# Performance work log

Measured on AMD Instinct MI355X. Metric: run time of the kernel, lower is better.

Reference implementation:

```python
import jax, jax.numpy as jnp
import numpy as np

V, E, G = 25000, 50000, 1024
D_IN, E_IN, D, EH = 74, 12, 64, 128
STEPS, S2S, L, NT = 6, 6, 3, 1


def setup_inputs() -> dict:
    key = jax.random.key(0)
    ks = jax.random.split(key, 20)
    p = lambda k, shp: (jax.random.normal(k, shp, jnp.float32) * 0.05)
    return {
        "node_feats": jax.random.normal(ks[0], (V, D_IN), jnp.float32),
        "edge_feats": jax.random.normal(ks[1], (E, E_IN), jnp.float32),
        "src": jax.random.randint(ks[2], (E,), 0, V),
        "dst": jax.random.randint(ks[3], (E,), 0, V),
        "node2graph": jnp.sort(jax.random.randint(ks[4], (V,), 0, G)),
        "W_proj": p(ks[5], (D_IN, D)), "b_proj": jnp.zeros((D,), jnp.float32),
        "W_e1": p(ks[6], (E_IN, EH)), "b_e1": jnp.zeros((EH,), jnp.float32),
        "W_e2": p(ks[7], (EH, D * D)), "b_e2": jnp.zeros((D * D,), jnp.float32),
        "b_conv": jnp.zeros((D,), jnp.float32),
        "gru_W_ih": p(ks[8], (3 * D, D)), "gru_W_hh": p(ks[9], (3 * D, D)),
        "gru_b_ih": jnp.zeros((3 * D,), jnp.float32), "gru_b_hh": jnp.zeros((3 * D,), jnp.float32),
        "lstm_W_ih0": p(ks[10], (4 * D, 2 * D)), "lstm_W_hh0": p(ks[11], (4 * D, D)),
        "lstm_b_ih0": jnp.zeros((4 * D,), jnp.float32), "lstm_b_hh0": jnp.zeros((4 * D,), jnp.float32),
        "lstm_W_ih_r": p(ks[12], (L - 1, 4 * D, D)), "lstm_W_hh_r": p(ks[13], (L - 1, 4 * D, D)),
        "lstm_b_ih_r": jnp.zeros((L - 1, 4 * D), jnp.float32), "lstm_b_hh_r": jnp.zeros((L - 1, 4 * D), jnp.float32),
        "W1": p(ks[14], (2 * D, D)), "b1": jnp.zeros((D,), jnp.float32),
        "bn_gamma": jnp.ones((D,), jnp.float32), "bn_beta": jnp.zeros((D,), jnp.float32),
        "bn_mean": jnp.zeros((D,), jnp.float32), "bn_var": jnp.ones((D,), jnp.float32),
        "W2": p(ks[15], (D, 4 * NT)), "b2": jnp.zeros((4 * NT,), jnp.float32),
    }


def reference(node_feats, edge_feats, src, dst, node2graph,
              W_proj, b_proj, W_e1, b_e1, W_e2, b_e2, b_conv,
              gru_W_ih, gru_W_hh, gru_b_ih, gru_b_hh,
              lstm_W_ih0, lstm_W_hh0, lstm_b_ih0, lstm_b_hh0,
              lstm_W_ih_r, lstm_W_hh_r, lstm_b_ih_r, lstm_b_hh_r,
              W1, b1, bn_gamma, bn_beta, bn_mean, bn_var, W2, b2):
    # --- MPNNGNN: project + ReLU, then NNConv(sum) + ReLU + GRU, x STEPS ---
    h = jax.nn.relu(node_feats @ W_proj + b_proj)                       # (V, D)
    # edge network: per-edge (D,D) mixing matrix (edge_feats constant across steps)
    We = (jax.nn.relu(edge_feats @ W_e1 + b_e1) @ W_e2 + b_e2).reshape(E, D, D)

    def mp_step(hh, _):
        m = jnp.einsum('ed,edo->eo', hh[src], We)                       # per-edge message
        agg = jax.ops.segment_sum(m, dst, num_segments=V) + b_conv      # NNConv sum + bias
        x = jax.nn.relu(agg)
        gi = x @ gru_W_ih.T + gru_b_ih                                  # GRU (torch gate order r,z,n)
        gh = hh @ gru_W_hh.T + gru_b_hh
        ir, iz, inn = jnp.split(gi, 3, axis=-1)
        hr, hz, hn = jnp.split(gh, 3, axis=-1)
        r = jax.nn.sigmoid(ir + hr)
        z = jax.nn.sigmoid(iz + hz)
        n = jnp.tanh(inn + r * hn)
        return (1.0 - z) * n + z * hh, None

    h, _ = jax.lax.scan(mp_step, h, None, length=STEPS)

    # --- Set2Set readout ---
    q_star = jnp.zeros((G, 2 * D), h.dtype)
    hs = jnp.zeros((L, G, D), h.dtype)
    cs = jnp.zeros((L, G, D), h.dtype)
    for _ in range(S2S):
        x = q_star
        nh, nc = [], []
        for l in range(L):                                              # stacked LSTM, seq len 1
            Wih = lstm_W_ih0 if l == 0 else lstm_W_ih_r[l - 1]
            Whh = lstm_W_hh0 if l == 0 else lstm_W_hh_r[l - 1]
            bih = lstm_b_ih0 if l == 0 else lstm_b_ih_r[l - 1]
            bhh = lstm_b_hh0 if l == 0 else lstm_b_hh_r[l - 1]
            gates = x @ Wih.T + bih + hs[l] @ Whh.T + bhh               # torch order i,f,g,o
            i, f, g, o = jnp.split(gates, 4, axis=-1)
            c = jax.nn.sigmoid(f) * cs[l] + jax.nn.sigmoid(i) * jnp.tanh(g)
            hc = jax.nn.sigmoid(o) * jnp.tanh(c)
            nh.append(hc); nc.append(c)
            x = hc
        hs, cs = jnp.stack(nh), jnp.stack(nc)
        q = x                                                           # (G, D)
        e = jnp.sum(h * q[node2graph], axis=-1)                         # (V,) attention logits
        emax = jax.lax.stop_gradient(jax.ops.segment_max(e, node2graph, num_segments=G))
        emax = jnp.where(jnp.isfinite(emax), emax, 0.0)
        ez = jnp.exp(e - emax[node2graph])                              # per-graph softmax
        denom = jax.ops.segment_sum(ez, node2graph, num_segments=G)
        alpha = ez / jnp.maximum(denom[node2graph], 1e-12)
        readout = jax.ops.segment_sum(h * alpha[:, None], node2graph, num_segments=G)
        q_star = jnp.concatenate([q, readout], axis=-1)                 # (G, 2D)

    # --- evidential head: Linear + ReLU + BatchNorm(eval) + Linear ---
    h1 = jax.nn.relu(q_star @ W1 + b1)
    hbn = bn_gamma * (h1 - bn_mean) * jax.lax.rsqrt(bn_var + 1e-5) + bn_beta
    out = hbn @ W2 + b2                                                 # (G, 4*NT)
    means, logl, loga, logb = jnp.split(out, 4, axis=1)
    MINV = 1e-6
    lam = jax.nn.softplus(logl) + MINV
    alp = jax.nn.softplus(loga) + MINV + 1.0
    bet = jax.nn.softplus(logb) + MINV
    return jnp.stack([means, lam, alp, bet], axis=2).reshape(out.shape)
```

## Files before the change

### kernel.cpp

```cpp
#include <hip/hip_runtime.h>
#include <stdint.h>

#define V_N 25000
#define E_N 50000
#define G_N 1024
#define DIN 74
#define EIN 12
#define NSTEPS 6
#define NS2S 6
#define MPAD 50176

typedef unsigned int u32;
typedef unsigned short u16;
typedef __attribute__((ext_vector_type(8))) short bf16x8v;
typedef __attribute__((ext_vector_type(4))) float f32x4v;

typedef __attribute__((address_space(3))) void lds_void;
typedef __attribute__((address_space(1))) void gbl_void;

__device__ __forceinline__ void gload_lds16(const void* g, void* l) {
  __builtin_amdgcn_global_load_lds((gbl_void*)g, (lds_void*)l, 16, 0, 0);
}

__device__ __forceinline__ u16 f2bf(float f) {
  u32 u = __float_as_uint(f);
  u = (u + 0x7fffu + ((u >> 16) & 1u)) >> 16;
  return (u16)u;
}
__device__ __forceinline__ u32 pack2bf(float lo, float hi) {
  return (u32)f2bf(lo) | ((u32)f2bf(hi) << 16);
}
__device__ __forceinline__ float bflo(u32 w){ return __uint_as_float(w << 16); }
__device__ __forceinline__ float bfhi(u32 w){ return __uint_as_float(w & 0xffff0000u); }
__device__ __forceinline__ float bf2f(u16 v){ return __uint_as_float(((u32)v) << 16); }
__device__ __forceinline__ float sigf(float x){ return 1.f/(1.f + expf(-x)); }
__device__ __forceinline__ float splusf(float x){ return fmaxf(x, 0.f) + log1pf(expf(-fabsf(x))); }

__global__ void prep_kernel(const float* gWih, const float* gWhh,
                            const float* lWih0, const float* lWhh0,
                            const float* lWihr, const float* lWhhr,
                            const float* We2,
                            float* gWihT, float* gWhhT,
                            u32* TW40, u32* TU40, u32* TW4r, u32* TU4r,
                            u16* WbT) {
  int idx = blockIdx.x * 256 + threadIdx.x;
  if (idx < 12288) { int d = idx / 192, r = idx % 192; gWihT[idx] = gWih[r*64 + d]; return; }
  idx -= 12288;
  if (idx < 12288) { int d = idx / 192, r = idx % 192; gWhhT[idx] = gWhh[r*64 + d]; return; }
  idx -= 12288;
  if (idx < 16384) { int q = idx >> 2, j = idx & 3; int k8 = q >> 8, r = q & 255;
                     TW40[idx] = pack2bf(lWih0[r*128 + k8*8 + 2*j], lWih0[r*128 + k8*8 + 2*j + 1]); return; }
  idx -= 16384;
  if (idx < 8192)  { int q = idx >> 2, j = idx & 3; int k8 = q >> 8, r = q & 255;
                     TU40[idx] = pack2bf(lWhh0[r*64 + k8*8 + 2*j], lWhh0[r*64 + k8*8 + 2*j + 1]); return; }
  idx -= 8192;
  if (idx < 16384) { int l = idx >> 13, rem = idx & 8191; int q = rem >> 2, j = rem & 3;
                     int k8 = q >> 8, r = q & 255;
                     TW4r[idx] = pack2bf(lWihr[l*16384 + r*64 + k8*8 + 2*j],
                                         lWihr[l*16384 + r*64 + k8*8 + 2*j + 1]); return; }
  idx -= 16384;
  if (idx < 16384) { int l = idx >> 13, rem = idx & 8191; int q = rem >> 2, j = rem & 3;
                     int k8 = q >> 8, r = q & 255;
                     TU4r[idx] = pack2bf(lWhhr[l*16384 + r*64 + k8*8 + 2*j],
                                         lWhhr[l*16384 + r*64 + k8*8 + 2*j + 1]); return; }
  idx -= 16384;
  { int n = idx / 128, k = idx % 128; WbT[idx] = f2bf(We2[k*4096 + n]); }
}

__global__ void proj_kernel(const float* nf, const float* Wp, const float* bp, float* h) {
  int v = blockIdx.x * 4 + (threadIdx.x >> 6);
  int o = threadIdx.x & 63;
  if (v >= V_N) return;
  float acc = bp[o];
  const float* row = nf + (size_t)v * DIN;
  #pragma unroll 2
  for (int d = 0; d < DIN; ++d) acc += row[d] * Wp[d*64 + o];
  h[(size_t)v*64 + o] = fmaxf(acc, 0.f);
}

__global__ void edgenet_kernel(const float* ef, const float* W1, const float* b1, u16* zb) {
  int e = blockIdx.x * 2 + (threadIdx.x >> 7);
  int k = threadIdx.x & 127;
  float acc = 0.f;
  if (e < E_N) {
    acc = b1[k];
    const float* row = ef + (size_t)e * EIN;
    #pragma unroll
    for (int i = 0; i < EIN; ++i) acc += row[i] * W1[i*128 + k];
    acc = fmaxf(acc, 0.f);
  }
  zb[(size_t)e*128 + k] = f2bf(acc);
}

__global__ __launch_bounds__(256) void fusedmsg_kernel(const u16* zb, const u16* WbT, const float* be2,
                                                       const float* h, const int* src, const int* dst,
                                                       float* agg) {
  __shared__ __align__(16) u16 Bs[2][8192];
  __shared__ u16 hS[128][66];
  __shared__ float beS[4096];
  int t = threadIdx.x;
  int e0 = blockIdx.x * 128;
  int w = t >> 6, lane = t & 63;
  int l16 = lane & 15, lh = lane >> 4;

  #pragma unroll
  for (int it = 0; it < 16; ++it) beS[it * 256 + t] = be2[it * 256 + t];

  for (int it = 0; it < 32; ++it) {
    int idx = it * 256 + t;
    int el = idx >> 6, d = idx & 63;
    int e = e0 + el;
    int sv = (e < E_N) ? src[e] : 0;
    hS[el][d] = f2bf(h[(size_t)sv * 64 + d]);
  }

  bf16x8v af[2][4];
  #pragma unroll
  for (int rf = 0; rf < 2; ++rf)
    #pragma unroll
    for (int ks = 0; ks < 4; ++ks)
      af[rf][ks] = *(const bf16x8v*)(zb + (size_t)(e0 + w*32 + rf*16 + l16)*128 + ks*32 + lh*8);

  {
    const char* Bg = (const char*)WbT;
    char* Bl = (char*)Bs[0];
    #pragma unroll
    for (int it = 0; it < 4; ++it) {
      int f = it * 256 + t;
      int r = f >> 4, s = f & 15;
      int gc = s ^ (r & 7);
      gload_lds16(Bg + r*256 + gc*16, Bl + (size_t)(f & ~63) * 16);
    }
  }
  __syncthreads();

  float macc[2][4][4];
  #pragma unroll
  for (int rf = 0; rf < 2; ++rf)
    #pragma unroll
    for (int of = 0; of < 4; ++of)
      #pragma unroll
      for (int r = 0; r < 4; ++r) macc[rf][of][r] = 0.f;

  for (int d = 0; d < 64; ++d) {
    int buf = d & 1;
    if (d < 63) {
      const char* Bg = (const char*)WbT + (size_t)(d + 1) * 16384;
      char* Bl = (char*)Bs[buf ^ 1];
      #pragma unroll
      for (int it = 0; it < 4; ++it) {
        int f = it * 256 + t;
        int r = f >> 4, s = f & 15;
        int gc = s ^ (r & 7);
        gload_lds16(Bg + r*256 + gc*16, Bl + (size_t)(f & ~63) * 16);
      }
    }
    float hv[2][4];
    #pragma unroll
    for (int rf = 0; rf < 2; ++rf)
      #pragma unroll
      for (int r = 0; r < 4; ++r)
        hv[rf][r] = bf2f(hS[w*32 + rf*16 + lh*4 + r][d]);

    const char* Bb = (const char*)Bs[buf];
    #pragma unroll
    for (int of = 0; of < 4; ++of) {
      float bias = beS[d*64 + of*16 + l16];
      f32x4v c0 = (f32x4v){bias, bias, bias, bias};
      f32x4v c1 = c0;
      #pragma unroll
      for (int ks = 0; ks < 4; ++ks) {
        int brow = of*16 + l16;
        int cb = ks*4 + lh;
        bf16x8v bf = *(const bf16x8v*)(Bb + brow*256 + ((cb ^ (brow & 7)) << 4));
        c0 = __builtin_amdgcn_mfma_f32_16x16x32_bf16(af[0][ks], bf, c0, 0, 0, 0);
        c1 = __builtin_amdgcn_mfma_f32_16x16x32_bf16(af[1][ks], bf, c1, 0, 0, 0);
      }
      #pragma unroll
      for (int r = 0; r < 4; ++r) {
        macc[0][of][r] += hv[0][r] * c0[r];
        macc[1][of][r] += hv[1][r] * c1[r];
      }
    }
    __syncthreads();
  }

  #pragma unroll
  for (int rf = 0; rf < 2; ++rf)
    #pragma unroll
    for (int r = 0; r < 4; ++r) {
      int row = w*32 + rf*16 + lh*4 + r;
      int e = e0 + row;
      if (e < E_N) {
        int dv = dst[e];
        #pragma unroll
        for (int of = 0; of < 4; ++of)
          atomicAdd(&agg[(size_t)dv*64 + of*16 + l16], macc[rf][of][r]);
      }
    }
}

__global__ void gru_kernel(const float* aggc, const float* bconv, const float* WihT, const float* WhhT,
                           const float* bih, const float* bhh, float* h, float* aggz) {
  int wbase = (blockIdx.x * 4 + (threadIdx.x >> 6)) * 4;
  int o = threadIdx.x & 63;
  float xv[4], hv[4];
  #pragma unroll
  for (int n = 0; n < 4; ++n) {
    int v = wbase + n;
    if (v < V_N) { xv[n] = fmaxf(aggc[(size_t)v*64 + o] + bconv[o], 0.f); hv[n] = h[(size_t)v*64 + o]; }
    else { xv[n] = 0.f; hv[n] = 0.f; }
  }
  float ar[4] = {0,0,0,0}, az[4] = {0,0,0,0}, an[4] = {0,0,0,0};
  float br[4] = {0,0,0,0}, bz[4] = {0,0,0,0}, bn2[4] = {0,0,0,0};
  #pragma unroll 4
  for (int d = 0; d < 64; ++d) {
    float wr = WihT[d*192 + o], wz = WihT[d*192 + 64 + o], wn = WihT[d*192 + 128 + o];
    float ur = WhhT[d*192 + o], uz = WhhT[d*192 + 64 + o], un = WhhT[d*192 + 128 + o];
    #pragma unroll
    for (int n = 0; n < 4; ++n) {
      float xd = __shfl(xv[n], d);
      float hd = __shfl(hv[n], d);
      ar[n] += xd*wr; az[n] += xd*wz; an[n] += xd*wn;
      br[n] += hd*ur; bz[n] += hd*uz; bn2[n] += hd*un;
    }
  }
  float b_r = bih[o] + bhh[o], b_z = bih[64+o] + bhh[64+o];
  float bin = bih[128+o], bhn = bhh[128+o];
  #pragma unroll
  for (int n = 0; n < 4; ++n) {
    int v = wbase + n;
    if (v >= V_N) continue;
    float r  = sigf(ar[n] + br[n] + b_r);
    float z  = sigf(az[n] + bz[n] + b_z);
    float nn = tanhf(an[n] + bin + r*(bn2[n] + bhn));
    h[(size_t)v*64 + o] = (1.f - z)*nn + z*hv[n];
    aggz[(size_t)v*64 + o] = 0.f;
  }
}

__global__ void gstart_kernel(const int* n2g, int* gstart) {
  int g = blockIdx.x * 256 + threadIdx.x;
  if (g > G_N) return;
  int lo = 0, hi = V_N;
  while (lo < hi) { int mid = (lo + hi) >> 1; if (n2g[mid] < g) lo = mid + 1; else hi = mid; }
  gstart[g] = lo;
}

__global__ __launch_bounds__(256) void s2s_kernel(const float* h, const int* gstart,
    const uint4* TW40, const uint4* TU40, const uint4* TW4r, const uint4* TU4r,
    const float* bih0, const float* bhh0, const float* bihr, const float* bhhr,
    float* qstar) {
  __shared__ float sq[2][128];
  __shared__ float sx[2][128];
  __shared__ float shs[2][3][64], scs[2][3][64];
  __shared__ float sg[2][256];
  __shared__ float sred[2][2][66];
  int tt = threadIdx.x;
  int g0blk = blockIdx.x * 2;
  int w = tt >> 6, lane = tt & 63;
  int gsl = w >> 1, wsub = w & 1;
  int nstart = gstart[g0blk + gsl], nend = gstart[g0blk + gsl + 1];

  if (tt < 256) { ((float*)sq)[tt] = 0.f; }
  for (int i = tt; i < 384; i += 256) { ((float*)shs)[i] = 0.f; ((float*)scs)[i] = 0.f; }
  __syncthreads();

  for (int iter = 0; iter < NS2S; ++iter) {
    ((float*)sx)[tt] = ((float*)sq)[tt];
    __syncthreads();

    for (int l = 0; l < 3; ++l) {
      const uint4* TW = (l == 0) ? TW40 : TW4r + (size_t)(l-1) * 2048;
      const uint4* TU = (l == 0) ? TU40 : TU4r + (size_t)(l-1) * 2048;
      const float* bi = (l == 0) ? bih0 : bihr + (l-1)*256;
      const float* bh = (l == 0) ? bhh0 : bhhr + (l-1)*256;
      float bsum = bi[tt] + bh[tt];
      float acc0 = bsum, acc1 = bsum;
      if (l == 0) {
        #pragma unroll
        for (int k8 = 0; k8 < 16; ++k8) {
          uint4 u = TW[k8*256 + tt];
          const float4 xa0 = *(const float4*)&sx[0][k8*8];
          const float4 xb0 = *(const float4*)&sx[0][k8*8 + 4];
          const float4 xa1 = *(const float4*)&sx[1][k8*8];
          const float4 xb1 = *(const float4*)&sx[1][k8*8 + 4];
          float w0=bflo(u.x),w1=bfhi(u.x),w2=bflo(u.y),w3=bfhi(u.y);
          float w4=bflo(u.z),w5=bfhi(u.z),w6=bflo(u.w),w7=bfhi(u.w);
          acc0 += xa0.x*w0 + xa0.y*w1 + xa0.z*w2 + xa0.w*w3
                + xb0.x*w4 + xb0.y*w5 + xb0.z*w6 + xb0.w*w7;
          acc1 += xa1.x*w0 + xa1.y*w1 + xa1.z*w2 + xa1.w*w3
                + xb1.x*w4 + xb1.y*w5 + xb1.z*w6 + xb1.w*w7;
        }
      } else {
        #pragma unroll
        for (int k8 = 0; k8 < 8; ++k8) {
          uint4 u = TW[k8*256 + tt];
          const float4 xa0 = *(const float4*)&sx[0][k8*8];
          const float4 xb0 = *(const float4*)&sx[0][k8*8 + 4];
          const float4 xa1 = *(const float4*)&sx[1][k8*8];
          const float4 xb1 = *(const float4*)&sx[1][k8*8 + 4];
          float w0=bflo(u.x),w1=bfhi(u.x),w2=bflo(u.y),w3=bfhi(u.y);
          float w4=bflo(u.z),w5=bfhi(u.z),w6=bflo(u.w),w7=bfhi(u.w);
          acc0 += xa0.x*w0 + xa0.y*w1 + xa0.z*w2 + xa0.w*w3
                + xb0.x*w4 + xb0.y*w5 + xb0.z*w6 + xb0.w*w7;
          acc1 += xa1.x*w0 + xa1.y*w1 + xa1.z*w2 + xa1.w*w3
                + xb1.x*w4 + xb1.y*w5 + xb1.z*w6 + xb1.w*w7;
        }
      }
      #pragma unroll
      for (int k8 = 0; k8 < 8; ++k8) {
        uint4 u = TU[k8*256 + tt];
        const float4 ha0 = *(const float4*)&shs[0][l][k8*8];
        const float4 hb0 = *(const float4*)&shs[0][l][k8*8 + 4];
        const float4 ha1 = *(const float4*)&shs[1][l][k8*8];
        const float4 hb1 = *(const float4*)&shs[1][l][k8*8 + 4];
        float w0=bflo(u.x),w1=bfhi(u.x),w2=bflo(u.y),w3=bfhi(u.y);
        float w4=bflo(u.z),w5=bfhi(u.z),w6=bflo(u.w),w7=bfhi(u.w);
        acc0 += ha0.x*w0 + ha0.y*w1 + ha0.z*w2 + ha0.w*w3
              + hb0.x*w4 + hb0.y*w5 + hb0.z*w6 + hb0.w*w7;
        acc1 += ha1.x*w0 + ha1.y*w1 + ha1.z*w2 + ha1.w*w3
              + hb1.x*w4 + hb1.y*w5 + hb1.z*w6 + hb1.w*w7;
      }
      sg[0][tt] = acc0; sg[1][tt] = acc1;
      __syncthreads();
      if (tt < 128) {
        int gq = tt >> 6, r = tt & 63;
        float gv_i = sg[gq][r], gv_f = sg[gq][64+r], gv_g = sg[gq][128+r], gv_o = sg[gq][192+r];
        float c = sigf(gv_f)*scs[gq][l][r] + sigf(gv_i)*tanhf(gv_g);
        float hc = sigf(gv_o)*tanhf(c);
        scs[gq][l][r] = c; shs[gq][l][r] = hc; sx[gq][r] = hc;
      }
      __syncthreads();
    }

    {
      float q_l = sx[gsl][lane];
      float lmax = -3.4e38f;
      int i = nstart + wsub;
      for (; i + 2 < nend; i += 4) {
        float h0 = h[(size_t)i*64 + lane];
        float h1 = h[(size_t)(i+2)*64 + lane];
        float v0 = h0 * q_l, v1 = h1 * q_l;
        #pragma unroll
        for (int off = 32; off; off >>= 1) { v0 += __shfl_xor(v0, off); v1 += __shfl_xor(v1, off); }
        lmax = fmaxf(lmax, fmaxf(v0, v1));
      }
      if (i < nend) {
        float h0 = h[(size_t)i*64 + lane];
        float v0 = h0 * q_l;
        #pragma unroll
        for (int off = 32; off; off >>= 1) v0 += __shfl_xor(v0, off);
        lmax = fmaxf(lmax, v0);
      }
      if (lane == 0) sred[gsl][wsub][64] = lmax;
      __syncthreads();
      float gmax = fmaxf(sred[gsl][0][64], sred[gsl][1][64]);
      float lsum = 0.f, accv = 0.f;
      i = nstart + wsub;
      for (; i + 2 < nend; i += 4) {
        float h0 = h[(size_t)i*64 + lane];
        float h1 = h[(size_t)(i+2)*64 + lane];
        float v0 = h0 * q_l, v1 = h1 * q_l;
        #pragma unroll
        for (int off = 32; off; off >>= 1) { v0 += __shfl_xor(v0, off); v1 += __shfl_xor(v1, off); }
        float e0 = expf(v0 - gmax), e1 = expf(v1 - gmax);
        lsum += e0 + e1; accv += e0*h0 + e1*h1;
      }
      if (i < nend) {
        float h0 = h[(size_t)i*64 + lane];
        float v0 = h0 * q_l;
        #pragma unroll
        for (int off = 32; off; off >>= 1) v0 += __shfl_xor(v0, off);
        float e0 = expf(v0 - gmax);
        lsum += e0; accv += e0*h0;
      }
      sred[gsl][wsub][lane] = accv;
      if (lane == 0) sred[gsl][wsub][65] = lsum;
      __syncthreads();
      if (tt < 128) {
        int gq = tt >> 6, r = tt & 63;
        float den = sred[gq][0][65] + sred[gq][1][65];
        float ro = (sred[gq][0][r] + sred[gq][1][r]) / fmaxf(den, 1e-12f);
        sq[gq][r] = sx[gq][r];
        sq[gq][64 + r] = ro;
      }
      __syncthreads();
    }
  }

  qstar[(size_t)g0blk * 128 + tt] = ((float*)sq)[tt];
}

__global__ void head_kernel(const float* qstar, const float* W1, const float* b1,
                            const float* gma, const float* gbe, const float* gme, const float* gva,
                            const float* W2, const float* b2, float* out) {
  __shared__ float hb[4][64];
  int wslot = threadIdx.x >> 6;
  int g = blockIdx.x * 4 + wslot;
  int o = threadIdx.x & 63;
  float acc = b1[o];
  const float* q = qstar + (size_t)g * 128;
  #pragma unroll 4
  for (int k = 0; k < 128; ++k) acc += q[k] * W1[k*64 + o];
  acc = fmaxf(acc, 0.f);
  float hbn = gma[o] * (acc - gme[o]) * rsqrtf(gva[o] + 1e-5f) + gbe[o];
  hb[wslot][o] = hbn;
  __syncthreads();
  if (o < 4) {
    float v = b2[o];
    #pragma unroll 8
    for (int k = 0; k < 64; ++k) v += hb[wslot][k] * W2[k*4 + o];
    float res;
    if (o == 0) res = v;
    else { res = splusf(v) + 1e-6f; if (o == 2) res += 1.f; }
    out[(size_t)g*4 + o] = res;
  }
}

extern "C" void kernel_launch(void* const* d_in, const int* in_sizes, int n_in,
                              void* d_out, int out_size, void* d_ws, size_t ws_size,
                              hipStream_t stream) {
  const float* node_feats = (const float*)d_in[0];
  const float* edge_feats = (const float*)d_in[1];
  const int*   src        = (const int*)d_in[2];
  const int*   dst        = (const int*)d_in[3];
  const int*   n2g        = (const int*)d_in[4];
  const float* W_proj = (const float*)d_in[5];
  const float* b_proj = (const float*)d_in[6];
  const float* W_e1   = (const float*)d_in[7];
  const float* b_e1   = (const float*)d_in[8];
  const float* W_e2   = (const float*)d_in[9];
  const float* b_e2   = (const float*)d_in[10];
  const float* b_conv = (const float*)d_in[11];
  const float* gru_W_ih = (const float*)d_in[12];
  const float* gru_W_hh = (const float*)d_in[13];
  const float* gru_b_ih = (const float*)d_in[14];
  const float* gru_b_hh = (const float*)d_in[15];
  const float* lstm_W_ih0 = (const float*)d_in[16];
  const float* lstm_W_hh0 = (const float*)d_in[17];
  const float* lstm_b_ih0 = (const float*)d_in[18];
  const float* lstm_b_hh0 = (const float*)d_in[19];
  const float* lstm_W_ih_r = (const float*)d_in[20];
  const float* lstm_W_hh_r = (const float*)d_in[21];
  const float* lstm_b_ih_r = (const float*)d_in[22];
  const float* lstm_b_hh_r = (const float*)d_in[23];
  const float* W1 = (const float*)d_in[24];
  const float* b1 = (const float*)d_in[25];
  const float* bn_gamma = (const float*)d_in[26];
  const float* bn_beta  = (const float*)d_in[27];
  const float* bn_mean  = (const float*)d_in[28];
  const float* bn_var   = (const float*)d_in[29];
  const float* W2 = (const float*)d_in[30];
  const float* b2 = (const float*)d_in[31];

  char* ws = (char*)d_ws;
  size_t off = 0;
  auto alloc = [&](size_t n) { size_t c = off; off += (n + 255) & ~(size_t)255; return c; };
  u16*   zb     = (u16*)  (ws + alloc((size_t)MPAD * 128 * 2));
  float* h      = (float*)(ws + alloc((size_t)V_N * 64 * 4));
  float* agg    = (float*)(ws + alloc((size_t)V_N * 64 * 4));
  u16*   WbT    = (u16*)  (ws + alloc((size_t)4096 * 128 * 2));
  float* gWihT  = (float*)(ws + alloc(12288 * 4));
  float* gWhhT  = (float*)(ws + alloc(12288 * 4));
  u32*   TW40   = (u32*)  (ws + alloc(16384 * 4));
  u32*   TU40   = (u32*)  (ws + alloc(8192 * 4));
  u32*   TW4r   = (u32*)  (ws + alloc(16384 * 4));
  u32*   TU4r   = (u32*)  (ws + alloc(16384 * 4));
  int*   gstart = (int*)  (ws + alloc(1025 * 4));
  float* qstar  = (float*)(ws + alloc((size_t)G_N * 128 * 4));
  (void)in_sizes; (void)n_in; (void)out_size; (void)ws_size;

  prep_kernel<<<2368, 256, 0, stream>>>(gru_W_ih, gru_W_hh, lstm_W_ih0, lstm_W_hh0,
                                        lstm_W_ih_r, lstm_W_hh_r, W_e2,
                                        gWihT, gWhhT, TW40, TU40, TW4r, TU4r, WbT);
  proj_kernel<<<6250, 256, 0, stream>>>(node_feats, W_proj, b_proj, h);
  edgenet_kernel<<<MPAD / 2, 256, 0, stream>>>(edge_feats, W_e1, b_e1, zb);
  hipMemsetAsync(agg, 0, (size_t)V_N * 64 * 4, stream);

  for (int st = 0; st < NSTEPS; ++st) {
    fusedmsg_kernel<<<MPAD / 128, 256, 0, stream>>>(zb, WbT, b_e2, h, src, dst, agg);
    gru_kernel<<<1563, 256, 0, stream>>>(agg, b_conv, gWihT, gWhhT, gru_b_ih, gru_b_hh, h, agg);
  }

  gstart_kernel<<<5, 256, 0, stream>>>(n2g, gstart);
  s2s_kernel<<<512, 256, 0, stream>>>(h, gstart, (const uint4*)TW40, (const uint4*)TU40,
                                      (const uint4*)TW4r, (const uint4*)TU4r,
                                      lstm_b_ih0, lstm_b_hh0, lstm_b_ih_r, lstm_b_hh_r, qstar);
  head_kernel<<<256, 256, 0, stream>>>(qstar, W1, b1, bn_gamma, bn_beta, bn_mean, bn_var,
                                       W2, b2, (float*)d_out);
}
```

Before: 1.140 ms.

## Rewrite Set2Set LSTM as single-wavefront-per-graph kernel with shuffle broadcasts

The Set2Set kernel now runs one 64-lane wavefront per graph instead of a 256-thread block covering two graphs. Each lane computes all four LSTM gates for its own hidden unit, so gate activations stay in registers. The input vector is broadcast with __shfl instead of through LDS, which removes every __syncthreads. LSTM weights are repacked in prep as gate-interleaved bf16 pairs indexed [k][o], and the biases are pre-summed. The trade-off is less parallelism for the attention loop over nodes and a longer serial chain of 64-step dot products per lane, which raises per-wave latency.

```diff
diff --git a/kernel.cpp b/kernel.cpp
--- a/kernel.cpp
+++ b/kernel.cpp
@@ -39,32 +39,59 @@
 __global__ void prep_kernel(const float* gWih, const float* gWhh,
                             const float* lWih0, const float* lWhh0,
                             const float* lWihr, const float* lWhhr,
+                            const float* lb_ih0, const float* lb_hh0,
+                            const float* lb_ihr, const float* lb_hhr,
                             const float* We2,
                             float* gWihT, float* gWhhT,
-                            u32* TW40, u32* TU40, u32* TW4r, u32* TU4r,
-                            u16* WbT) {
+                            uint2* T0W, uint2* T0U, uint2* TrW, uint2* TrU,
+                            float4* bs4, u16* WbT) {
   int idx = blockIdx.x * 256 + threadIdx.x;
   if (idx < 12288) { int d = idx / 192, r = idx % 192; gWihT[idx] = gWih[r*64 + d]; return; }
   idx -= 12288;
   if (idx < 12288) { int d = idx / 192, r = idx % 192; gWhhT[idx] = gWhh[r*64 + d]; return; }
   idx -= 12288;
-  if (idx < 16384) { int q = idx >> 2, j = idx & 3; int k8 = q >> 8, r = q & 255;
-                     TW40[idx] = pack2bf(lWih0[r*128 + k8*8 + 2*j], lWih0[r*128 + k8*8 + 2*j + 1]); return; }
-  idx -= 16384;
-  if (idx < 8192)  { int q = idx >> 2, j = idx & 3; int k8 = q >> 8, r = q & 255;
-                     TU40[idx] = pack2bf(lWhh0[r*64 + k8*8 + 2*j], lWhh0[r*64 + k8*8 + 2*j + 1]); return; }
+  if (idx < 8192) {
+    int k = idx >> 6, o = idx & 63;
+    T0W[idx] = (uint2){ pack2bf(lWih0[o*128 + k],        lWih0[(64+o)*128 + k]),
+                        pack2bf(lWih0[(128+o)*128 + k],  lWih0[(192+o)*128 + k]) };
+    return;
+  }
   idx -= 8192;
-  if (idx < 16384) { int l = idx >> 13, rem = idx & 8191; int q = rem >> 2, j = rem & 3;
-                     int k8 = q >> 8, r = q & 255;
-                     TW4r[idx] = pack2bf(lWihr[l*16384 + r*64 + k8*8 + 2*j],
-                                         lWihr[l*16384 + r*64 + k8*8 + 2*j + 1]); return; }
-  idx -= 16384;
-  if (idx < 16384) { int l = idx >> 13, rem = idx & 8191; int q = rem >> 2, j = rem & 3;
-                     int k8 = q >> 8, r = q & 255;
-                     TU4r[idx] = pack2bf(lWhhr[l*16384 + r*64 + k8*8 + 2*j],
-                                         lWhhr[l*16384 + r*64 + k8*8 + 2*j + 1]); return; }
-  idx -= 16384;
-  { int n = idx / 128, k = idx % 128; WbT[idx] = f2bf(We2[k*4096 + n]); }
+  if (idx < 4096) {
+    int k = idx >> 6, o = idx & 63;
+    T0U[idx] = (uint2){ pack2bf(lWhh0[o*64 + k],        lWhh0[(64+o)*64 + k]),
+                        pack2bf(lWhh0[(128+o)*64 + k],  lWhh0[(192+o)*64 + k]) };
+    return;
+  }
+  idx -= 4096;
+  if (idx < 8192) {
+    int l = idx >> 12, rem = idx & 4095;
+    int k = rem >> 6, o = rem & 63;
+    const float* W = lWihr + l*16384;
+    TrW[idx] = (uint2){ pack2bf(W[o*64 + k],        W[(64+o)*64 + k]),
+                        pack2bf(W[(128+o)*64 + k],  W[(192+o)*64 + k]) };
+    return;
+  }
+  idx -= 8192;
+  if (idx < 8192) {
+    int l = idx >> 12, rem = idx & 4095;
+    int k = rem >> 6, o = rem & 63;
+    const float* W = lWhhr + l*16384;
+    TrU[idx] = (uint2){ pack2bf(W[o*64 + k],        W[(64+o)*64 + k]),
+                        pack2bf(W[(128+o)*64 + k],  W[(192+o)*64 + k]) };
+    return;
+  }
+  idx -= 8192;
+  if (idx < 192) {
+    int l = idx >> 6, o = idx & 63;
+    const float* bi = (l == 0) ? lb_ih0 : lb_ihr + (l-1)*256;
+    const float* bh = (l == 0) ? lb_hh0 : lb_hhr + (l-1)*256;
+    bs4[idx] = (float4){ bi[o] + bh[o], bi[64+o] + bh[64+o],
+                         bi[128+o] + bh[128+o], bi[192+o] + bh[192+o] };
+    return;
+  }
+  idx -= 192;
+  if (idx < 524288) { int n = idx / 128, k = idx % 128; WbT[idx] = f2bf(We2[k*4096 + n]); }
 }
 
 __global__ void proj_kernel(const float* nf, const float* Wp, const float* bp, float* h) {
@@ -247,149 +274,119 @@
   gstart[g] = lo;
 }
 
-__global__ __launch_bounds__(256) void s2s_kernel(const float* h, const int* gstart,
-    const uint4* TW40, const uint4* TU40, const uint4* TW4r, const uint4* TU4r,
-    const float* bih0, const float* bhh0, const float* bihr, const float* bhhr,
-    float* qstar) {
-  __shared__ float sq[2][128];
-  __shared__ float sx[2][128];
-  __shared__ float shs[2][3][64], scs[2][3][64];
-  __shared__ float sg[2][256];
-  __shared__ float sred[2][2][66];
-  int tt = threadIdx.x;
-  int g0blk = blockIdx.x * 2;
-  int w = tt >> 6, lane = tt & 63;
-  int gsl = w >> 1, wsub = w & 1;
-  int nstart = gstart[g0blk + gsl], nend = gstart[g0blk + gsl + 1];
-
-  if (tt < 256) { ((float*)sq)[tt] = 0.f; }
-  for (int i = tt; i < 384; i += 256) { ((float*)shs)[i] = 0.f; ((float*)scs)[i] = 0.f; }
-  __syncthreads();
+__global__ __launch_bounds__(64) void s2s_kernel(const float* h, const int* gstart,
+    const uint2* T0W, const uint2* T0U, const uint2* TrW, const uint2* TrU,
+    const float4* bs4, float* qstar) {
+  int lane = threadIdx.x;
+  int g = blockIdx.x;
+  int ns = gstart[g], ne = gstart[g + 1];
+  float xq = 0.f, xr = 0.f;
+  float hs0 = 0.f, hs1 = 0.f, hs2 = 0.f;
+  float cs0 = 0.f, cs1 = 0.f, cs2 = 0.f;
 
   for (int iter = 0; iter < NS2S; ++iter) {
-    ((float*)sx)[tt] = ((float*)sq)[tt];
-    __syncthreads();
-
-    for (int l = 0; l < 3; ++l) {
-      const uint4* TW = (l == 0) ? TW40 : TW4r + (size_t)(l-1) * 2048;
-      const uint4* TU = (l == 0) ? TU40 : TU4r + (size_t)(l-1) * 2048;
-      const float* bi = (l == 0) ? bih0 : bihr + (l-1)*256;
-      const float* bh = (l == 0) ? bhh0 : bhhr + (l-1)*256;
-      float bsum = bi[tt] + bh[tt];
-      float acc0 = bsum, acc1 = bsum;
-      if (l == 0) {
-        #pragma unroll
-        for (int k8 = 0; k8 < 16; ++k8) {
-          uint4 u = TW[k8*256 + tt];
-          const float4 xa0 = *(const float4*)&sx[0][k8*8];
-          const float4 xb0 = *(const float4*)&sx[0][k8*8 + 4];
-          const float4 xa1 = *(const float4*)&sx[1][k8*8];
-          const float4 xb1 = *(const float4*)&sx[1][k8*8 + 4];
-          float w0=bflo(u.x),w1=bfhi(u.x),w2=bflo(u.y),w3=bfhi(u.y);
-          float w4=bflo(u.z),w5=bfhi(u.z),w6=bflo(u.w),w7=bfhi(u.w);
-          acc0 += xa0.x*w0 + xa0.y*w1 + xa0.z*w2 + xa0.w*w3
-                + xb0.x*w4 + xb0.y*w5 + xb0.z*w6 + xb0.w*w7;
-          acc1 += xa1.x*w0 + xa1.y*w1 + xa1.z*w2 + xa1.w*w3
-                + xb1.x*w4 + xb1.y*w5 + xb1.z*w6 + xb1.w*w7;
-        }
-      } else {
-        #pragma unroll
-        for (int k8 = 0; k8 < 8; ++k8) {
-          uint4 u = TW[k8*256 + tt];
-          const float4 xa0 = *(const float4*)&sx[0][k8*8];
-          const float4 xb0 = *(const float4*)&sx[0][k8*8 + 4];
-          const float4 xa1 = *(const float4*)&sx[1][k8*8];
-          const float4 xb1 = *(const float4*)&sx[1][k8*8 + 4];
-          float w0=bflo(u.x),w1=bfhi(u.x),w2=bflo(u.y),w3=bfhi(u.y);
-          float w4=bflo(u.z),w5=bfhi(u.z),w6=bflo(u.w),w7=bfhi(u.w);
-          acc0 += xa0.x*w0 + xa0.y*w1 + xa0.z*w2 + xa0.w*w3
-                + xb0.x*w4 + xb0.y*w5 + xb0.z*w6 + xb0.w*w7;
-          acc1 += xa1.x*w0 + xa1.y*w1 + xa1.z*w2 + xa1.w*w3
-                + xb1.x*w4 + xb1.y*w5 + xb1.z*w6 + xb1.w*w7;
-        }
-      }
-      #pragma unroll
-      for (int k8 = 0; k8 < 8; ++k8) {
-        uint4 u = TU[k8*256 + tt];
-        const float4 ha0 = *(const float4*)&shs[0][l][k8*8];
-        const float4 hb0 = *(const float4*)&shs[0][l][k8*8 + 4];
-        const float4 ha1 = *(const float4*)&shs[1][l][k8*8];
-        const float4 hb1 = *(const float4*)&shs[1][l][k8*8 + 4];
-        float w0=bflo(u.x),w1=bfhi(u.x),w2=bflo(u.y),w3=bfhi(u.y);
-        float w4=bflo(u.z),w5=bfhi(u.z),w6=bflo(u.w),w7=bfhi(u.w);
-        acc0 += ha0.x*w0 + ha0.y*w1 + ha0.z*w2 + ha0.w*w3
-              + hb0.x*w4 + hb0.y*w5 + hb0.z*w6 + hb0.w*w7;
-        acc1 += ha1.x*w0 + ha1.y*w1 + ha1.z*w2 + ha1.w*w3
-              + hb1.x*w4 + hb1.y*w5 + hb1.z*w6 + hb1.w*w7;
-      }
-      sg[0][tt] = acc0; sg[1][tt] = acc1;
-      __syncthreads();
-      if (tt < 128) {
-        int gq = tt >> 6, r = tt & 63;
-        float gv_i = sg[gq][r], gv_f = sg[gq][64+r], gv_g = sg[gq][128+r], gv_o = sg[gq][192+r];
-        float c = sigf(gv_f)*scs[gq][l][r] + sigf(gv_i)*tanhf(gv_g);
-        float hc = sigf(gv_o)*tanhf(c);
-        scs[gq][l][r] = c; shs[gq][l][r] = hc; sx[gq][r] = hc;
-      }
-      __syncthreads();
-    }
-
-    {
-      float q_l = sx[gsl][lane];
-      float lmax = -3.4e38f;
-      int i = nstart + wsub;
-      for (; i + 2 < nend; i += 4) {
-        float h0 = h[(size_t)i*64 + lane];
-        float h1 = h[(size_t)(i+2)*64 + lane];
-        float v0 = h0 * q_l, v1 = h1 * q_l;
-        #pragma unroll
-        for (int off = 32; off; off >>= 1) { v0 += __shfl_xor(v0, off); v1 += __shfl_xor(v1, off); }
-        lmax = fmaxf(lmax, fmaxf(v0, v1));
-      }
-      if (i < nend) {
-        float h0 = h[(size_t)i*64 + lane];
-        float v0 = h0 * q_l;
-        #pragma unroll
-        for (int off = 32; off; off >>= 1) v0 += __shfl_xor(v0, off);
-        lmax = fmaxf(lmax, v0);
-      }
-      if (lane == 0) sred[gsl][wsub][64] = lmax;
-      __syncthreads();
-      float gmax = fmaxf(sred[gsl][0][64], sred[gsl][1][64]);
-      float lsum = 0.f, accv = 0.f;
-      i = nstart + wsub;
-      for (; i + 2 < nend; i += 4) {
-        float h0 = h[(size_t)i*64 + lane];
-        float h1 = h[(size_t)(i+2)*64 + lane];
-        float v0 = h0 * q_l, v1 = h1 * q_l;
-        #pragma unroll
-        for (int off = 32; off; off >>= 1) { v0 += __shfl_xor(v0, off); v1 += __shfl_xor(v1, off); }
-        float e0 = expf(v0 - gmax), e1 = expf(v1 - gmax);
-        lsum += e0 + e1; accv += e0*h0 + e1*h1;
-      }
-      if (i < nend) {
-        float h0 = h[(size_t)i*64 + lane];
-        float v0 = h0 * q_l;
-        #pragma unroll
-        for (int off = 32; off; off >>= 1) v0 += __shfl_xor(v0, off);
-        float e0 = expf(v0 - gmax);
-        lsum += e0; accv += e0*h0;
-      }
-      sred[gsl][wsub][lane] = accv;
-      if (lane == 0) sred[gsl][wsub][65] = lsum;
-      __syncthreads();
-      if (tt < 128) {
-        int gq = tt >> 6, r = tt & 63;
-        float den = sred[gq][0][65] + sred[gq][1][65];
-        float ro = (sred[gq][0][r] + sred[gq][1][r]) / fmaxf(den, 1e-12f);
-        sq[gq][r] = sx[gq][r];
-        sq[gq][64 + r] = ro;
-      }
-      __syncthreads();
-    }
-  }
-
-  qstar[(size_t)g0blk * 128 + tt] = ((float*)sq)[tt];
+    float4 bv = bs4[lane];
+    float a0 = bv.x, a1 = bv.y, a2 = bv.z, a3 = bv.w;
+    #pragma unroll 16
+    for (int k = 0; k < 64; ++k) {
+      uint2 u = T0W[k*64 + lane];
+      float xk = __shfl(xq, k);
+      a0 += xk*bflo(u.x); a1 += xk*bfhi(u.x); a2 += xk*bflo(u.y); a3 += xk*bfhi(u.y);
+    }
+    #pragma unroll 16
+    for (int k = 0; k < 64; ++k) {
+      uint2 u = T0W[(64 + k)*64 + lane];
+      float xk = __shfl(xr, k);
+      a0 += xk*bflo(u.x); a1 += xk*bfhi(u.x); a2 += xk*bflo(u.y); a3 += xk*bfhi(u.y);
+    }
+    #pragma unroll 16
+    for (int k = 0; k < 64; ++k) {
+      uint2 u = T0U[k*64 + lane];
+      float hk = __shfl(hs0, k);
+      a0 += hk*bflo(u.x); a1 += hk*bfhi(u.x); a2 += hk*bflo(u.y); a3 += hk*bfhi(u.y);
+    }
+    float c0v = sigf(a1)*cs0 + sigf(a0)*tanhf(a2);
+    float x1 = sigf(a3)*tanhf(c0v);
+    cs0 = c0v; hs0 = x1;
+
+    bv = bs4[64 + lane];
+    a0 = bv.x; a1 = bv.y; a2 = bv.z; a3 = bv.w;
+    #pragma unroll 16
+    for (int k = 0; k < 64; ++k) {
+      uint2 u = TrW[k*64 + lane];
+      float xk = __shfl(x1, k);
+      a0 += xk*bflo(u.x); a1 += xk*bfhi(u.x); a2 += xk*bflo(u.y); a3 += xk*bfhi(u.y);
+    }
+    #pragma unroll 16
+    for (int k = 0; k < 64; ++k) {
+      uint2 u = TrU[k*64 + lane];
+      float hk = __shfl(hs1, k);
+      a0 += hk*bflo(u.x); a1 += hk*bfhi(u.x); a2 += hk*bflo(u.y); a3 += hk*bfhi(u.y);
+    }
+    float c1v = sigf(a1)*cs1 + sigf(a0)*tanhf(a2);
+    float x2 = sigf(a3)*tanhf(c1v);
+    cs1 = c1v; hs1 = x2;
+
+    bv = bs4[128 + lane];
+    a0 = bv.x; a1 = bv.y; a2 = bv.z; a3 = bv.w;
+    #pragma unroll 16
+    for (int k = 0; k < 64; ++k) {
+      uint2 u = TrW[4096 + k*64 + lane];
+      float xk = __shfl(x2, k);
+      a0 += xk*bflo(u.x); a1 += xk*bfhi(u.x); a2 += xk*bflo(u.y); a3 += xk*bfhi(u.y);
+    }
+    #pragma unroll 16
+    for (int k = 0; k < 64; ++k) {
+      uint2 u = TrU[4096 + k*64 + lane];
+      float hk = __shfl(hs2, k);
+      a0 += hk*bflo(u.x); a1 += hk*bfhi(u.x); a2 += hk*bflo(u.y); a3 += hk*bfhi(u.y);
+    }
+    float c2v = sigf(a1)*cs2 + sigf(a0)*tanhf(a2);
+    float qv = sigf(a3)*tanhf(c2v);
+    cs2 = c2v; hs2 = qv;
+
+    float lmax = -3.4e38f;
+    int i = ns;
+    for (; i + 1 < ne; i += 2) {
+      float h0 = h[(size_t)i*64 + lane];
+      float h1 = h[(size_t)(i+1)*64 + lane];
+      float v0 = h0 * qv, v1 = h1 * qv;
+      #pragma unroll
+      for (int off = 32; off; off >>= 1) { v0 += __shfl_xor(v0, off); v1 += __shfl_xor(v1, off); }
+      lmax = fmaxf(lmax, fmaxf(v0, v1));
+    }
+    if (i < ne) {
+      float h0 = h[(size_t)i*64 + lane];
+      float v0 = h0 * qv;
+      #pragma unroll
+      for (int off = 32; off; off >>= 1) v0 += __shfl_xor(v0, off);
+      lmax = fmaxf(lmax, v0);
+    }
+    float lsum = 0.f, accv = 0.f;
+    i = ns;
+    for (; i + 1 < ne; i += 2) {
+      float h0 = h[(size_t)i*64 + lane];
+      float h1 = h[(size_t)(i+1)*64 + lane];
+      float v0 = h0 * qv, v1 = h1 * qv;
+      #pragma unroll
+      for (int off = 32; off; off >>= 1) { v0 += __shfl_xor(v0, off); v1 += __shfl_xor(v1, off); }
+      float e0 = expf(v0 - lmax), e1 = expf(v1 - lmax);
+      lsum += e0 + e1; accv += e0*h0 + e1*h1;
+    }
+    if (i < ne) {
+      float h0 = h[(size_t)i*64 + lane];
+      float v0 = h0 * qv;
+      #pragma unroll
+      for (int off = 32; off; off >>= 1) v0 += __shfl_xor(v0, off);
+      float e0 = expf(v0 - lmax);
+      lsum += e0; accv += e0*h0;
+    }
+    xq = qv;
+    xr = accv / fmaxf(lsum, 1e-12f);
+  }
+
+  qstar[(size_t)g*128 + lane] = xq;
+  qstar[(size_t)g*128 + 64 + lane] = xr;
 }
 
 __global__ void head_kernel(const float* qstar, const float* W1, const float* b1,
@@ -457,23 +454,25 @@
   char* ws = (char*)d_ws;
   size_t off = 0;
   auto alloc = [&](size_t n) { size_t c = off; off += (n + 255) & ~(size_t)255; return c; };
-  u16*   zb     = (u16*)  (ws + alloc((size_t)MPAD * 128 * 2));
-  float* h      = (float*)(ws + alloc((size_t)V_N * 64 * 4));
-  float* agg    = (float*)(ws + alloc((size_t)V_N * 64 * 4));
-  u16*   WbT    = (u16*)  (ws + alloc((size_t)4096 * 128 * 2));
-  float* gWihT  = (float*)(ws + alloc(12288 * 4));
-  float* gWhhT  = (float*)(ws + alloc(12288 * 4));
-  u32*   TW40   = (u32*)  (ws + alloc(16384 * 4));
-  u32*   TU40   = (u32*)  (ws + alloc(8192 * 4));
-  u32*   TW4r   = (u32*)  (ws + alloc(16384 * 4));
-  u32*   TU4r   = (u32*)  (ws + alloc(16384 * 4));
-  int*   gstart = (int*)  (ws + alloc(1025 * 4));
-  float* qstar  = (float*)(ws + alloc((size_t)G_N * 128 * 4));
+  u16*    zb     = (u16*)   (ws + alloc((size_t)MPAD * 128 * 2));
+  float*  h      = (float*) (ws + alloc((size_t)V_N * 64 * 4));
+  float*  agg    = (float*) (ws + alloc((size_t)V_N * 64 * 4));
+  u16*    WbT    = (u16*)   (ws + alloc((size_t)4096 * 128 * 2));
+  float*  gWihT  = (float*) (ws + alloc(12288 * 4));
+  float*  gWhhT  = (float*) (ws + alloc(12288 * 4));
+  uint2*  T0W    = (uint2*) (ws + alloc(8192 * 8));
+  uint2*  T0U    = (uint2*) (ws + alloc(4096 * 8));
+  uint2*  TrW    = (uint2*) (ws + alloc(8192 * 8));
+  uint2*  TrU    = (uint2*) (ws + alloc(8192 * 8));
+  float4* bs4    = (float4*)(ws + alloc(192 * 16));
+  int*    gstart = (int*)   (ws + alloc(1025 * 4));
+  float*  qstar  = (float*) (ws + alloc((size_t)G_N * 128 * 4));
   (void)in_sizes; (void)n_in; (void)out_size; (void)ws_size;
 
-  prep_kernel<<<2368, 256, 0, stream>>>(gru_W_ih, gru_W_hh, lstm_W_ih0, lstm_W_hh0,
-                                        lstm_W_ih_r, lstm_W_hh_r, W_e2,
-                                        gWihT, gWhhT, TW40, TU40, TW4r, TU4r, WbT);
+  prep_kernel<<<2257, 256, 0, stream>>>(gru_W_ih, gru_W_hh, lstm_W_ih0, lstm_W_hh0,
+                                        lstm_W_ih_r, lstm_W_hh_r,
+                                        lstm_b_ih0, lstm_b_hh0, lstm_b_ih_r, lstm_b_hh_r,
+                                        W_e2, gWihT, gWhhT, T0W, T0U, TrW, TrU, bs4, WbT);
   proj_kernel<<<6250, 256, 0, stream>>>(node_feats, W_proj, b_proj, h);
   edgenet_kernel<<<MPAD / 2, 256, 0, stream>>>(edge_feats, W_e1, b_e1, zb);
   hipMemsetAsync(agg, 0, (size_t)V_N * 64 * 4, stream);
@@ -484,9 +483,7 @@
   }
 
   gstart_kernel<<<5, 256, 0, stream>>>(n2g, gstart);
-  s2s_kernel<<<512, 256, 0, stream>>>(h, gstart, (const uint4*)TW40, (const uint4*)TU40,
-                                      (const uint4*)TW4r, (const uint4*)TU4r,
-                                      lstm_b_ih0, lstm_b_hh0, lstm_b_ih_r, lstm_b_hh_r, qstar);
+  s2s_kernel<<<G_N, 64, 0, stream>>>(h, gstart, T0W, T0U, TrW, TrU, bs4, qstar);
   head_kernel<<<256, 256, 0, stream>>>(qstar, W1, b1, bn_gamma, bn_beta, bn_mean, bn_var,
                                        W2, b2, (float*)d_out);
 }
```

Result: slower. 1.168 ms (+2.4%).
